# Performance work log

Hardware: AMD Instinct MI355X
Metric: run time of the kernel (lower is better)

The kernel has to match this reference:

```python
import jax, jax.numpy as jnp
import numpy as np

# DeepSeek-V3 MoE config (matches init_kwargs)
H = 1024          # hidden_size
I = 704           # moe_intermediate_size
E = 64            # n_routed_experts
TOP_K = 8         # num_experts_per_tok
NG = 8            # n_group
TOPK_GROUP = 4    # topk_group
N_SHARED = 2      # n_shared_experts
ROUTED_SCALE = 2.5
S_I = I * N_SHARED  # shared expert intermediate size


def setup_inputs() -> dict:
    key = jax.random.key(0)
    ks = jax.random.split(key, 10)
    sc = 0.02
    return {
        "hidden_states": jax.random.normal(ks[0], (1, 1024, H), dtype=jnp.float32),
        "gate_w": sc * jax.random.normal(ks[1], (E, H), dtype=jnp.float32),
        "gate_bias": sc * jax.random.normal(ks[2], (E,), dtype=jnp.float32),  # e_score_correction_bias
        "Wg": sc * jax.random.normal(ks[3], (E, I, H), dtype=jnp.float32),
        "Wu": sc * jax.random.normal(ks[4], (E, I, H), dtype=jnp.float32),
        "Wd": sc * jax.random.normal(ks[5], (E, H, I), dtype=jnp.float32),
        "Sg": sc * jax.random.normal(ks[6], (S_I, H), dtype=jnp.float32),
        "Su": sc * jax.random.normal(ks[7], (S_I, H), dtype=jnp.float32),
        "Sd": sc * jax.random.normal(ks[8], (H, S_I), dtype=jnp.float32),
    }


def _route(x, gate_w, gate_bias):
    # x: [T, H] -> dense routing weight matrix [T, E]
    T = x.shape[0]
    logits = x @ gate_w.T                         # [T, E] (fp32, as HF casts to float32)
    scores = jax.nn.sigmoid(logits)
    scores_for_choice = scores + gate_bias[None, :]
    # group scores: sum of top-2 expert scores in each group
    grp = scores_for_choice.reshape(T, NG, E // NG)
    group_scores = jnp.sum(jax.lax.top_k(grp, 2)[0], axis=-1)      # [T, NG]
    _, gidx = jax.lax.top_k(group_scores, TOPK_GROUP)              # [T, TOPK_GROUP]
    gmask = jnp.zeros((T, NG), dtype=scores.dtype).at[
        jnp.arange(T)[:, None], gidx].set(1.0)                      # [T, NG]
    emask = jnp.repeat(gmask, E // NG, axis=1)                      # [T, E]
    masked = jnp.where(emask > 0, scores_for_choice, 0.0)
    _, topk_idx = jax.lax.top_k(masked, TOP_K)                      # [T, TOP_K]
    topk_w = jnp.take_along_axis(scores, topk_idx, axis=1)          # gather from UNbiased scores
    topk_w = topk_w / (jnp.sum(topk_w, axis=-1, keepdims=True) + 1e-20)  # norm_topk_prob
    topk_w = topk_w * ROUTED_SCALE
    # dense [T, E] combine weights (zeros for unrouted experts)
    rw = jnp.zeros((T, E), dtype=scores.dtype).at[
        jnp.arange(T)[:, None], topk_idx].add(topk_w)
    return rw


def _mlp(x, gw, uw, dw):
    # SwiGLU MLP: down(silu(gate(x)) * up(x)), no biases
    return (jax.nn.silu(x @ gw.T) * (x @ uw.T)) @ dw.T


def reference(hidden_states, gate_w, gate_bias, Wg, Wu, Wd, Sg, Su, Sd):
    B, S, _ = hidden_states.shape
    x = hidden_states.reshape(B * S, H)                 # [T, H]
    rw = _route(x, gate_w, gate_bias)                   # [T, E]
    # dense reference: run every expert on every token, weighted combine
    expert_out = jax.vmap(lambda gw_, uw_, dw_: _mlp(x, gw_, uw_, dw_))(Wg, Wu, Wd)  # [E, T, H]
    routed = jnp.einsum('eth,te->th', expert_out, rw)   # [T, H]
    shared = _mlp(x, Sg, Su, Sd)                        # [T, H]
    out = (routed + shared).reshape(B, S, H)
    return out
```

## Files before the change

### kernel.cpp

```cpp
#include <hip/hip_runtime.h>
#include <hip/hip_bf16.h>
#include <cstdint>
#include <cstddef>

#define T_TOK 1024
#define H_DIM 1024
#define I_DIM 704
#define E_NUM 64
#define TOPK 8
#define NGRP 8
#define GSIZE 8
#define TOPKG 4
#define SI_DIM 1408
#define RSCALE 2.5f
#define NSLOT (T_TOK * TOPK)
#define MAXBLK 128

#define AP 72

typedef short bf16x8 __attribute__((ext_vector_type(8)));
typedef float f32x4 __attribute__((ext_vector_type(4)));

__device__ inline unsigned pk2(float x, float y) {
    __hip_bfloat162 h2 = __float22bfloat162_rn(make_float2(x, y));
    unsigned u; __builtin_memcpy(&u, &h2, 4); return u;
}
__device__ inline unsigned short bf1(float x) {
    __hip_bfloat16 h = __float2bfloat16(x);
    unsigned short u; __builtin_memcpy(&u, &h, 2); return u;
}

__global__ __launch_bounds__(64) void route_kernel(
    const float* __restrict__ x, const float* __restrict__ gw, const float* __restrict__ gb,
    int* __restrict__ counts, int* __restrict__ tk_idx, float* __restrict__ tk_w)
{
    const int t = blockIdx.x;
    __shared__ float xs[H_DIM];
    __shared__ float raw[E_NUM];
    __shared__ float sc[E_NUM];
    __shared__ float masked[E_NUM];
    __shared__ float gsc[NGRP];
    const int tid = threadIdx.x;

    const float4* xrow = (const float4*)(x + (size_t)t * H_DIM);
    for (int i = tid; i < H_DIM / 4; i += 64) ((float4*)xs)[i] = xrow[i];
    __syncthreads();

    float a = 0.f;
    const float* w = gw + (size_t)tid * H_DIM;
    for (int h = 0; h < H_DIM; h += 4) {
        float4 w4 = *(const float4*)(w + h);
        a += xs[h] * w4.x + xs[h+1] * w4.y + xs[h+2] * w4.z + xs[h+3] * w4.w;
    }
    float s = 1.f / (1.f + expf(-a));
    raw[tid] = s;
    sc[tid] = s + gb[tid];
    __syncthreads();

    if (tid == 0) {
        for (int g = 0; g < NGRP; ++g) {
            float m1 = -1e30f, m2 = -1e30f;
            for (int j = 0; j < GSIZE; ++j) {
                float v = sc[g * GSIZE + j];
                if (v > m1) { m2 = m1; m1 = v; }
                else if (v > m2) { m2 = v; }
            }
            gsc[g] = m1 + m2;
        }
        bool gsel[NGRP];
        for (int g = 0; g < NGRP; ++g) gsel[g] = false;
        for (int k = 0; k < TOPKG; ++k) {
            int best = -1; float bv = -1e30f;
            for (int g = 0; g < NGRP; ++g)
                if (!gsel[g] && gsc[g] > bv) { bv = gsc[g]; best = g; }
            gsel[best] = true;
        }
        for (int e = 0; e < E_NUM; ++e)
            masked[e] = gsel[e / GSIZE] ? sc[e] : 0.0f;
        int idx[TOPK];
        float wsum = 0.f;
        for (int k = 0; k < TOPK; ++k) {
            int best = 0; float bv = -1e30f;
            for (int e = 0; e < E_NUM; ++e)
                if (masked[e] > bv) { bv = masked[e]; best = e; }
            masked[best] = -1e30f;
            idx[k] = best;
            wsum += raw[best];
        }
        float inv = RSCALE / (wsum + 1e-20f);
        for (int k = 0; k < TOPK; ++k) {
            tk_idx[t * TOPK + k] = idx[k];
            tk_w[t * TOPK + k] = raw[idx[k]] * inv;
            atomicAdd(&counts[idx[k]], 1);
        }
    }
}

__global__ void zero_kernel(int* counts, int* fillc)
{
    int i = threadIdx.x;
    if (i < E_NUM) { counts[i] = 0; fillc[i] = 0; }
}

__global__ void scan_kernel(const int* __restrict__ counts, int* __restrict__ offs,
                            int* __restrict__ blk_e, int* __restrict__ blk_s0,
                            int* __restrict__ nblk)
{
    if (threadIdx.x == 0) {
        int acc = 0;
        for (int e = 0; e < E_NUM; ++e) { offs[e] = acc; acc += counts[e]; }
        int n = 0;
        for (int e = 0; e < E_NUM; ++e)
            for (int t = 0; t < counts[e]; t += 128) { blk_e[n] = e; blk_s0[n] = t; ++n; }
        nblk[0] = n;
    }
}

__global__ void fill_kernel(const int* __restrict__ tk_idx, const float* __restrict__ tk_w,
                            const int* __restrict__ offs, int* __restrict__ fillc,
                            int* __restrict__ tok_list, float* __restrict__ w_list,
                            int* __restrict__ tk_pos)
{
    int t = blockIdx.x * blockDim.x + threadIdx.x;
    if (t >= T_TOK) return;
    for (int k = 0; k < TOPK; ++k) {
        int e = tk_idx[t * TOPK + k];
        int pos = offs[e] + atomicAdd(&fillc[e], 1);
        tok_list[pos] = t;
        w_list[pos] = tk_w[t * TOPK + k];
        tk_pos[t * TOPK + k] = pos;
    }
}

__global__ __launch_bounds__(256) void gateup_routed_mfma(
    const float* __restrict__ x, const float* __restrict__ Wg, const float* __restrict__ Wu,
    const int* __restrict__ offs, const int* __restrict__ counts,
    const int* __restrict__ tok_list, const float* __restrict__ w_list,
    const int* __restrict__ blk_e, const int* __restrict__ blk_s0, const int* __restrict__ nblk,
    unsigned short* __restrict__ act)
{
    const int by = blockIdx.y;
    if (by >= nblk[0]) return;
    const int e = blk_e[by];
    const int m0 = blk_s0[by];
    const int cnt = counts[e];
    const int off = offs[e];
    const int n0 = blockIdx.x * 64;

    __shared__ unsigned short As[128 * AP];
    __shared__ unsigned short Bg[64 * AP];
    __shared__ unsigned short Bu[64 * AP];
    __shared__ int toks[128];
    __shared__ float wts[128];

    const int tid = threadIdx.x;
    if (tid < 128) {
        int s = m0 + tid;
        toks[tid] = (s < cnt) ? tok_list[off + s] : -1;
        wts[tid]  = (s < cnt) ? w_list[off + s] : 0.f;
    }
    __syncthreads();

    const int lane = tid & 63;
    const int wv = tid >> 6;
    const int lr = lane & 15;
    const int lq = lane >> 4;

    f32x4 accg[2][4], accu[2][4];
    #pragma unroll
    for (int i = 0; i < 2; ++i)
        #pragma unroll
        for (int j = 0; j < 4; ++j) {
            accg[i][j] = (f32x4){0.f, 0.f, 0.f, 0.f};
            accu[i][j] = (f32x4){0.f, 0.f, 0.f, 0.f};
        }

    const float* wgp = Wg + (size_t)e * I_DIM * H_DIM + (size_t)n0 * H_DIM;
    const float* wup = Wu + (size_t)e * I_DIM * H_DIM + (size_t)n0 * H_DIM;

    const int ar = tid >> 4;
    const int ac = (tid & 15) * 4;

    for (int k0 = 0; k0 < H_DIM; k0 += 64) {
        #pragma unroll
        for (int p = 0; p < 8; ++p) {
            int r = ar + p * 16;
            int tkn = toks[r];
            float4 v = make_float4(0.f, 0.f, 0.f, 0.f);
            if (tkn >= 0) v = *(const float4*)(x + (size_t)tkn * H_DIM + k0 + ac);
            *(uint2*)&As[r * AP + ac] = make_uint2(pk2(v.x, v.y), pk2(v.z, v.w));
        }
        #pragma unroll
        for (int p = 0; p < 4; ++p) {
            int r = ar + p * 16;
            float4 g = *(const float4*)(wgp + (size_t)r * H_DIM + k0 + ac);
            *(uint2*)&Bg[r * AP + ac] = make_uint2(pk2(g.x, g.y), pk2(g.z, g.w));
            float4 u = *(const float4*)(wup + (size_t)r * H_DIM + k0 + ac);
            *(uint2*)&Bu[r * AP + ac] = make_uint2(pk2(u.x, u.y), pk2(u.z, u.w));
        }
        __syncthreads();
        #pragma unroll
        for (int ks = 0; ks < 2; ++ks) {
            bf16x8 a0 = *(const bf16x8*)&As[(wv * 32 + lr) * AP + ks * 32 + lq * 8];
            bf16x8 a1 = *(const bf16x8*)&As[(wv * 32 + 16 + lr) * AP + ks * 32 + lq * 8];
            #pragma unroll
            for (int nj = 0; nj < 4; ++nj) {
                bf16x8 bg = *(const bf16x8*)&Bg[(nj * 16 + lr) * AP + ks * 32 + lq * 8];
                bf16x8 bu = *(const bf16x8*)&Bu[(nj * 16 + lr) * AP + ks * 32 + lq * 8];
                accg[0][nj] = __builtin_amdgcn_mfma_f32_16x16x32_bf16(a0, bg, accg[0][nj], 0, 0, 0);
                accg[1][nj] = __builtin_amdgcn_mfma_f32_16x16x32_bf16(a1, bg, accg[1][nj], 0, 0, 0);
                accu[0][nj] = __builtin_amdgcn_mfma_f32_16x16x32_bf16(a0, bu, accu[0][nj], 0, 0, 0);
                accu[1][nj] = __builtin_amdgcn_mfma_f32_16x16x32_bf16(a1, bu, accu[1][nj], 0, 0, 0);
            }
        }
        __syncthreads();
    }

    #pragma unroll
    for (int mi = 0; mi < 2; ++mi) {
        #pragma unroll
        for (int r = 0; r < 4; ++r) {
            int srow = wv * 32 + mi * 16 + lq * 4 + r;
            if (m0 + srow < cnt) {
                float w = wts[srow];
                unsigned short* ap = act + (size_t)(off + m0 + srow) * I_DIM + n0 + lr;
                #pragma unroll
                for (int nj = 0; nj < 4; ++nj) {
                    float g = accg[mi][nj][r];
                    float u = accu[mi][nj][r];
                    float a = w * (g / (1.f + __expf(-g))) * u;
                    ap[nj * 16] = bf1(a);
                }
            }
        }
    }
}

__global__ __launch_bounds__(256) void down_routed_mfma(
    const unsigned short* __restrict__ act, const float* __restrict__ Wd,
    const int* __restrict__ offs, const int* __restrict__ counts,
    const int* __restrict__ blk_e, const int* __restrict__ blk_s0, const int* __restrict__ nblk,
    float* __restrict__ slot_out)
{
    const int by = blockIdx.y;
    if (by >= nblk[0]) return;
    const int e = blk_e[by];
    const int m0 = blk_s0[by];
    const int cnt = counts[e];
    const int off = offs[e];
    const int n0 = blockIdx.x * 64;

    __shared__ unsigned short As[128 * AP];
    __shared__ unsigned short Bs[64 * AP];

    const int tid = threadIdx.x;
    const int lane = tid & 63;
    const int wv = tid >> 6;
    const int lr = lane & 15;
    const int lq = lane >> 4;

    f32x4 acc[2][4];
    #pragma unroll
    for (int i = 0; i < 2; ++i)
        #pragma unroll
        for (int j = 0; j < 4; ++j)
            acc[i][j] = (f32x4){0.f, 0.f, 0.f, 0.f};

    const float* wdp = Wd + (size_t)e * H_DIM * I_DIM + (size_t)n0 * I_DIM;
    const unsigned short* ap0 = act + (size_t)(off + m0) * I_DIM;
    const int ar = tid >> 4;
    const int ac = (tid & 15) * 4;

    for (int k0 = 0; k0 < I_DIM; k0 += 64) {
        #pragma unroll
        for (int p = 0; p < 8; ++p) {
            int r = ar + p * 16;
            uint2 v = make_uint2(0u, 0u);
            if (m0 + r < cnt) v = *(const uint2*)(ap0 + (size_t)r * I_DIM + k0 + ac);
            *(uint2*)&As[r * AP + ac] = v;
        }
        #pragma unroll
        for (int p = 0; p < 4; ++p) {
            int r = ar + p * 16;
            float4 w4 = *(const float4*)(wdp + (size_t)r * I_DIM + k0 + ac);
            *(uint2*)&Bs[r * AP + ac] = make_uint2(pk2(w4.x, w4.y), pk2(w4.z, w4.w));
        }
        __syncthreads();
        #pragma unroll
        for (int ks = 0; ks < 2; ++ks) {
            bf16x8 a0 = *(const bf16x8*)&As[(wv * 32 + lr) * AP + ks * 32 + lq * 8];
            bf16x8 a1 = *(const bf16x8*)&As[(wv * 32 + 16 + lr) * AP + ks * 32 + lq * 8];
            #pragma unroll
            for (int nj = 0; nj < 4; ++nj) {
                bf16x8 b = *(const bf16x8*)&Bs[(nj * 16 + lr) * AP + ks * 32 + lq * 8];
                acc[0][nj] = __builtin_amdgcn_mfma_f32_16x16x32_bf16(a0, b, acc[0][nj], 0, 0, 0);
                acc[1][nj] = __builtin_amdgcn_mfma_f32_16x16x32_bf16(a1, b, acc[1][nj], 0, 0, 0);
            }
        }
        __syncthreads();
    }

    #pragma unroll
    for (int mi = 0; mi < 2; ++mi) {
        #pragma unroll
        for (int r = 0; r < 4; ++r) {
            int srow = wv * 32 + mi * 16 + lq * 4 + r;
            if (m0 + srow < cnt) {
                float* op = slot_out + (size_t)(off + m0 + srow) * H_DIM + n0 + lr;
                #pragma unroll
                for (int nj = 0; nj < 4; ++nj)
                    op[nj * 16] = acc[mi][nj][r];
            }
        }
    }
}

__global__ __launch_bounds__(256) void combine_kernel(
    const float* __restrict__ slot_out, const int* __restrict__ tk_pos,
    float* __restrict__ out)
{
    const int t = blockIdx.x;
    __shared__ int pos[TOPK];
    if (threadIdx.x < TOPK) pos[threadIdx.x] = tk_pos[t * TOPK + threadIdx.x];
    __syncthreads();
    const int i = threadIdx.x;
    float4 a = ((const float4*)(out + (size_t)t * H_DIM))[i];
    #pragma unroll
    for (int k = 0; k < TOPK; ++k) {
        float4 v = ((const float4*)(slot_out + (size_t)pos[k] * H_DIM))[i];
        a.x += v.x; a.y += v.y; a.z += v.z; a.w += v.w;
    }
    ((float4*)(out + (size_t)t * H_DIM))[i] = a;
}

__global__ __launch_bounds__(256) void gateup_shared_mfma(
    const float* __restrict__ x, const float* __restrict__ Sg, const float* __restrict__ Su,
    unsigned short* __restrict__ sact)
{
    const int m0 = blockIdx.y * 128;
    const int n0 = blockIdx.x * 64;

    __shared__ unsigned short As[128 * AP];
    __shared__ unsigned short Bg[64 * AP];
    __shared__ unsigned short Bu[64 * AP];

    const int tid = threadIdx.x;
    const int lane = tid & 63;
    const int wv = tid >> 6;
    const int lr = lane & 15;
    const int lq = lane >> 4;

    f32x4 accg[2][4], accu[2][4];
    #pragma unroll
    for (int i = 0; i < 2; ++i)
        #pragma unroll
        for (int j = 0; j < 4; ++j) {
            accg[i][j] = (f32x4){0.f, 0.f, 0.f, 0.f};
            accu[i][j] = (f32x4){0.f, 0.f, 0.f, 0.f};
        }

    const float* gp = Sg + (size_t)n0 * H_DIM;
    const float* up = Su + (size_t)n0 * H_DIM;
    const int ar = tid >> 4;
    const int ac = (tid & 15) * 4;

    for (int k0 = 0; k0 < H_DIM; k0 += 64) {
        #pragma unroll
        for (int p = 0; p < 8; ++p) {
            int r = ar + p * 16;
            float4 v = *(const float4*)(x + (size_t)(m0 + r) * H_DIM + k0 + ac);
            *(uint2*)&As[r * AP + ac] = make_uint2(pk2(v.x, v.y), pk2(v.z, v.w));
        }
        #pragma unroll
        for (int p = 0; p < 4; ++p) {
            int r = ar + p * 16;
            float4 g = *(const float4*)(gp + (size_t)r * H_DIM + k0 + ac);
            *(uint2*)&Bg[r * AP + ac] = make_uint2(pk2(g.x, g.y), pk2(g.z, g.w));
            float4 u = *(const float4*)(up + (size_t)r * H_DIM + k0 + ac);
            *(uint2*)&Bu[r * AP + ac] = make_uint2(pk2(u.x, u.y), pk2(u.z, u.w));
        }
        __syncthreads();
        #pragma unroll
        for (int ks = 0; ks < 2; ++ks) {
            bf16x8 a0 = *(const bf16x8*)&As[(wv * 32 + lr) * AP + ks * 32 + lq * 8];
            bf16x8 a1 = *(const bf16x8*)&As[(wv * 32 + 16 + lr) * AP + ks * 32 + lq * 8];
            #pragma unroll
            for (int nj = 0; nj < 4; ++nj) {
                bf16x8 bg = *(const bf16x8*)&Bg[(nj * 16 + lr) * AP + ks * 32 + lq * 8];
                bf16x8 bu = *(const bf16x8*)&Bu[(nj * 16 + lr) * AP + ks * 32 + lq * 8];
                accg[0][nj] = __builtin_amdgcn_mfma_f32_16x16x32_bf16(a0, bg, accg[0][nj], 0, 0, 0);
                accg[1][nj] = __builtin_amdgcn_mfma_f32_16x16x32_bf16(a1, bg, accg[1][nj], 0, 0, 0);
                accu[0][nj] = __builtin_amdgcn_mfma_f32_16x16x32_bf16(a0, bu, accu[0][nj], 0, 0, 0);
                accu[1][nj] = __builtin_amdgcn_mfma_f32_16x16x32_bf16(a1, bu, accu[1][nj], 0, 0, 0);
            }
        }
        __syncthreads();
    }

    #pragma unroll
    for (int mi = 0; mi < 2; ++mi) {
        #pragma unroll
        for (int r = 0; r < 4; ++r) {
            int trow = m0 + wv * 32 + mi * 16 + lq * 4 + r;
            unsigned short* sp = sact + (size_t)trow * SI_DIM + n0 + lr;
            #pragma unroll
            for (int nj = 0; nj < 4; ++nj) {
                float g = accg[mi][nj][r];
                float u = accu[mi][nj][r];
                float a = (g / (1.f + __expf(-g))) * u;
                sp[nj * 16] = bf1(a);
            }
        }
    }
}

__global__ __launch_bounds__(256) void down_shared_mfma(
    const unsigned short* __restrict__ sact, const float* __restrict__ Sd,
    float* __restrict__ out)
{
    const int m0 = blockIdx.y * 128;
    const int n0 = blockIdx.x * 64;

    __shared__ unsigned short As[128 * AP];
    __shared__ unsigned short Bs[64 * AP];

    const int tid = threadIdx.x;
    const int lane = tid & 63;
    const int wv = tid >> 6;
    const int lr = lane & 15;
    const int lq = lane >> 4;

    f32x4 acc[2][4];
    #pragma unroll
    for (int i = 0; i < 2; ++i)
        #pragma unroll
        for (int j = 0; j < 4; ++j)
            acc[i][j] = (f32x4){0.f, 0.f, 0.f, 0.f};

    const float* wp = Sd + (size_t)n0 * SI_DIM;
    const int ar = tid >> 4;
    const int ac = (tid & 15) * 4;

    for (int k0 = 0; k0 < SI_DIM; k0 += 64) {
        #pragma unroll
        for (int p = 0; p < 8; ++p) {
            int r = ar + p * 16;
            uint2 v = *(const uint2*)(sact + (size_t)(m0 + r) * SI_DIM + k0 + ac);
            *(uint2*)&As[r * AP + ac] = v;
        }
        #pragma unroll
        for (int p = 0; p < 4; ++p) {
            int r = ar + p * 16;
            float4 w4 = *(const float4*)(wp + (size_t)r * SI_DIM + k0 + ac);
            *(uint2*)&Bs[r * AP + ac] = make_uint2(pk2(w4.x, w4.y), pk2(w4.z, w4.w));
        }
        __syncthreads();
        #pragma unroll
        for (int ks = 0; ks < 2; ++ks) {
            bf16x8 a0 = *(const bf16x8*)&As[(wv * 32 + lr) * AP + ks * 32 + lq * 8];
            bf16x8 a1 = *(const bf16x8*)&As[(wv * 32 + 16 + lr) * AP + ks * 32 + lq * 8];
            #pragma unroll
            for (int nj = 0; nj < 4; ++nj) {
                bf16x8 b = *(const bf16x8*)&Bs[(nj * 16 + lr) * AP + ks * 32 + lq * 8];
                acc[0][nj] = __builtin_amdgcn_mfma_f32_16x16x32_bf16(a0, b, acc[0][nj], 0, 0, 0);
                acc[1][nj] = __builtin_amdgcn_mfma_f32_16x16x32_bf16(a1, b, acc[1][nj], 0, 0, 0);
            }
        }
        __syncthreads();
    }

    #pragma unroll
    for (int mi = 0; mi < 2; ++mi) {
        #pragma unroll
        for (int r = 0; r < 4; ++r) {
            int trow = m0 + wv * 32 + mi * 16 + lq * 4 + r;
            float* op = out + (size_t)trow * H_DIM + n0 + lr;
            #pragma unroll
            for (int nj = 0; nj < 4; ++nj)
                op[nj * 16] = acc[mi][nj][r];
        }
    }
}

extern "C" void kernel_launch(void* const* d_in, const int* in_sizes, int n_in,
                              void* d_out, int out_size, void* d_ws, size_t ws_size,
                              hipStream_t stream)
{
    const float* x  = (const float*)d_in[0];
    const float* gw = (const float*)d_in[1];
    const float* gb = (const float*)d_in[2];
    const float* Wg = (const float*)d_in[3];
    const float* Wu = (const float*)d_in[4];
    const float* Wd = (const float*)d_in[5];
    const float* Sg = (const float*)d_in[6];
    const float* Su = (const float*)d_in[7];
    const float* Sd = (const float*)d_in[8];
    float* out = (float*)d_out;

    float* slot_out = (float*)d_ws;
    unsigned short* act  = (unsigned short*)(slot_out + (size_t)NSLOT * H_DIM);
    unsigned short* sact = act + (size_t)NSLOT * I_DIM;
    int* counts   = (int*)(sact + (size_t)T_TOK * SI_DIM);
    int* fillc    = counts + 64;
    int* offs     = fillc + 64;
    int* tk_idx   = offs + 64;
    float* tk_w   = (float*)(tk_idx + NSLOT);
    int* tok_list = (int*)(tk_w + NSLOT);
    float* w_list = (float*)(tok_list + NSLOT);
    int* tk_pos   = (int*)(w_list + NSLOT);
    int* blk_e    = tk_pos + NSLOT;
    int* blk_s0   = blk_e + MAXBLK;
    int* nblk     = blk_s0 + MAXBLK;

    zero_kernel<<<1, 64, 0, stream>>>(counts, fillc);
    route_kernel<<<T_TOK, 64, 0, stream>>>(x, gw, gb, counts, tk_idx, tk_w);
    scan_kernel<<<1, 64, 0, stream>>>(counts, offs, blk_e, blk_s0, nblk);
    fill_kernel<<<4, 256, 0, stream>>>(tk_idx, tk_w, offs, fillc, tok_list, w_list, tk_pos);

    gateup_routed_mfma<<<dim3(11, MAXBLK), 256, 0, stream>>>(
        x, Wg, Wu, offs, counts, tok_list, w_list, blk_e, blk_s0, nblk, act);
    gateup_shared_mfma<<<dim3(22, 8), 256, 0, stream>>>(x, Sg, Su, sact);
    down_shared_mfma<<<dim3(16, 8), 256, 0, stream>>>(sact, Sd, out);
    down_routed_mfma<<<dim3(16, MAXBLK), 256, 0, stream>>>(
        act, Wd, offs, counts, blk_e, blk_s0, nblk, slot_out);
    combine_kernel<<<T_TOK, 256, 0, stream>>>(slot_out, tk_pos, out);
}
```

Baseline: 808.2 us.

## Fold shared expert into routed grouped GEMM as two virtual experts

Treats the shared expert MLP as two extra virtual experts, each taking one half of the 1408 intermediate size and every token with weight 1. The shared expert then runs inside the same grouped gate/up and down kernels, and its outputs are summed in the combine kernel, which removes two separate launches. The GEMM blocks also grow from 256 to 512 threads, with each wave computing a 16-row slice instead of 32. This adds slot_out and act workspace for 2048 extra slots, and it adds extra reads in combine.

```diff
diff --git a/kernel.cpp b/kernel.cpp
--- a/kernel.cpp
+++ b/kernel.cpp
@@ -14,7 +14,9 @@
 #define SI_DIM 1408
 #define RSCALE 2.5f
 #define NSLOT (T_TOK * TOPK)
-#define MAXBLK 128
+#define NSLOT2 (NSLOT + 2 * T_TOK)
+#define EV_NUM (E_NUM + 2)
+#define MAXBLK 160
 
 #define AP 72
 
@@ -100,6 +102,7 @@
 {
     int i = threadIdx.x;
     if (i < E_NUM) { counts[i] = 0; fillc[i] = 0; }
+    if (i >= E_NUM && i < EV_NUM) counts[i] = T_TOK;
 }
 
 __global__ void scan_kernel(const int* __restrict__ counts, int* __restrict__ offs,
@@ -109,8 +112,10 @@
     if (threadIdx.x == 0) {
         int acc = 0;
         for (int e = 0; e < E_NUM; ++e) { offs[e] = acc; acc += counts[e]; }
+        offs[E_NUM]     = NSLOT;
+        offs[E_NUM + 1] = NSLOT + T_TOK;
         int n = 0;
-        for (int e = 0; e < E_NUM; ++e)
+        for (int e = 0; e < EV_NUM; ++e)
             for (int t = 0; t < counts[e]; t += 128) { blk_e[n] = e; blk_s0[n] = t; ++n; }
         nblk[0] = n;
     }
@@ -130,10 +135,13 @@
         w_list[pos] = tk_w[t * TOPK + k];
         tk_pos[t * TOPK + k] = pos;
     }
-}
-
-__global__ __launch_bounds__(256) void gateup_routed_mfma(
+    tok_list[NSLOT + t] = t;          w_list[NSLOT + t] = 1.f;
+    tok_list[NSLOT + T_TOK + t] = t;  w_list[NSLOT + T_TOK + t] = 1.f;
+}
+
+__global__ __launch_bounds__(512) void gateup_mfma(
     const float* __restrict__ x, const float* __restrict__ Wg, const float* __restrict__ Wu,
+    const float* __restrict__ Sg, const float* __restrict__ Su,
     const int* __restrict__ offs, const int* __restrict__ counts,
     const int* __restrict__ tok_list, const float* __restrict__ w_list,
     const int* __restrict__ blk_e, const int* __restrict__ blk_s0, const int* __restrict__ nblk,
@@ -166,33 +174,35 @@
     const int lr = lane & 15;
     const int lq = lane >> 4;
 
-    f32x4 accg[2][4], accu[2][4];
-    #pragma unroll
-    for (int i = 0; i < 2; ++i)
-        #pragma unroll
-        for (int j = 0; j < 4; ++j) {
-            accg[i][j] = (f32x4){0.f, 0.f, 0.f, 0.f};
-            accu[i][j] = (f32x4){0.f, 0.f, 0.f, 0.f};
-        }
-
-    const float* wgp = Wg + (size_t)e * I_DIM * H_DIM + (size_t)n0 * H_DIM;
-    const float* wup = Wu + (size_t)e * I_DIM * H_DIM + (size_t)n0 * H_DIM;
+    f32x4 accg[4], accu[4];
+    #pragma unroll
+    for (int j = 0; j < 4; ++j) {
+        accg[j] = (f32x4){0.f, 0.f, 0.f, 0.f};
+        accu[j] = (f32x4){0.f, 0.f, 0.f, 0.f};
+    }
+
+    const float* wgp = (e < E_NUM)
+        ? Wg + (size_t)e * I_DIM * H_DIM + (size_t)n0 * H_DIM
+        : Sg + (size_t)(e - E_NUM) * I_DIM * H_DIM + (size_t)n0 * H_DIM;
+    const float* wup = (e < E_NUM)
+        ? Wu + (size_t)e * I_DIM * H_DIM + (size_t)n0 * H_DIM
+        : Su + (size_t)(e - E_NUM) * I_DIM * H_DIM + (size_t)n0 * H_DIM;
 
     const int ar = tid >> 4;
     const int ac = (tid & 15) * 4;
 
     for (int k0 = 0; k0 < H_DIM; k0 += 64) {
         #pragma unroll
-        for (int p = 0; p < 8; ++p) {
-            int r = ar + p * 16;
+        for (int p = 0; p < 4; ++p) {
+            int r = ar + p * 32;
             int tkn = toks[r];
             float4 v = make_float4(0.f, 0.f, 0.f, 0.f);
             if (tkn >= 0) v = *(const float4*)(x + (size_t)tkn * H_DIM + k0 + ac);
             *(uint2*)&As[r * AP + ac] = make_uint2(pk2(v.x, v.y), pk2(v.z, v.w));
         }
         #pragma unroll
-        for (int p = 0; p < 4; ++p) {
-            int r = ar + p * 16;
+        for (int p = 0; p < 2; ++p) {
+            int r = ar + p * 32;
             float4 g = *(const float4*)(wgp + (size_t)r * H_DIM + k0 + ac);
             *(uint2*)&Bg[r * AP + ac] = make_uint2(pk2(g.x, g.y), pk2(g.z, g.w));
             float4 u = *(const float4*)(wup + (size_t)r * H_DIM + k0 + ac);
@@ -201,43 +211,38 @@
         __syncthreads();
         #pragma unroll
         for (int ks = 0; ks < 2; ++ks) {
-            bf16x8 a0 = *(const bf16x8*)&As[(wv * 32 + lr) * AP + ks * 32 + lq * 8];
-            bf16x8 a1 = *(const bf16x8*)&As[(wv * 32 + 16 + lr) * AP + ks * 32 + lq * 8];
+            bf16x8 a = *(const bf16x8*)&As[(wv * 16 + lr) * AP + ks * 32 + lq * 8];
             #pragma unroll
             for (int nj = 0; nj < 4; ++nj) {
                 bf16x8 bg = *(const bf16x8*)&Bg[(nj * 16 + lr) * AP + ks * 32 + lq * 8];
                 bf16x8 bu = *(const bf16x8*)&Bu[(nj * 16 + lr) * AP + ks * 32 + lq * 8];
-                accg[0][nj] = __builtin_amdgcn_mfma_f32_16x16x32_bf16(a0, bg, accg[0][nj], 0, 0, 0);
-                accg[1][nj] = __builtin_amdgcn_mfma_f32_16x16x32_bf16(a1, bg, accg[1][nj], 0, 0, 0);
-                accu[0][nj] = __builtin_amdgcn_mfma_f32_16x16x32_bf16(a0, bu, accu[0][nj], 0, 0, 0);
-                accu[1][nj] = __builtin_amdgcn_mfma_f32_16x16x32_bf16(a1, bu, accu[1][nj], 0, 0, 0);
+                accg[nj] = __builtin_amdgcn_mfma_f32_16x16x32_bf16(a, bg, accg[nj], 0, 0, 0);
+                accu[nj] = __builtin_amdgcn_mfma_f32_16x16x32_bf16(a, bu, accu[nj], 0, 0, 0);
             }
         }
         __syncthreads();
     }
 
     #pragma unroll
-    for (int mi = 0; mi < 2; ++mi) {
-        #pragma unroll
-        for (int r = 0; r < 4; ++r) {
-            int srow = wv * 32 + mi * 16 + lq * 4 + r;
-            if (m0 + srow < cnt) {
-                float w = wts[srow];
-                unsigned short* ap = act + (size_t)(off + m0 + srow) * I_DIM + n0 + lr;
-                #pragma unroll
-                for (int nj = 0; nj < 4; ++nj) {
-                    float g = accg[mi][nj][r];
-                    float u = accu[mi][nj][r];
-                    float a = w * (g / (1.f + __expf(-g))) * u;
-                    ap[nj * 16] = bf1(a);
-                }
+    for (int r = 0; r < 4; ++r) {
+        int srow = wv * 16 + lq * 4 + r;
+        if (m0 + srow < cnt) {
+            float w = wts[srow];
+            unsigned short* ap = act + (size_t)(off + m0 + srow) * I_DIM + n0 + lr;
+            #pragma unroll
+            for (int nj = 0; nj < 4; ++nj) {
+                float g = accg[nj][r];
+                float u = accu[nj][r];
+                float a = w * (g / (1.f + __expf(-g))) * u;
+                ap[nj * 16] = bf1(a);
             }
         }
     }
 }
 
-__global__ __launch_bounds__(256) void down_routed_mfma(
+__global__ __launch_bounds__(512) void down_mfma(
     const unsigned short* __restrict__ act, const float* __restrict__ Wd,
+    const float* __restrict__ Sd,
     const int* __restrict__ offs, const int* __restrict__ counts,
     const int* __restrict__ blk_e, const int* __restrict__ blk_s0, const int* __restrict__ nblk,
     float* __restrict__ slot_out)
@@ -259,58 +264,59 @@
     const int lr = lane & 15;
     const int lq = lane >> 4;
 
-    f32x4 acc[2][4];
-    #pragma unroll
-    for (int i = 0; i < 2; ++i)
-        #pragma unroll
-        for (int j = 0; j < 4; ++j)
-            acc[i][j] = (f32x4){0.f, 0.f, 0.f, 0.f};
-
-    const float* wdp = Wd + (size_t)e * H_DIM * I_DIM + (size_t)n0 * I_DIM;
+    f32x4 acc[4];
+    #pragma unroll
+    for (int j = 0; j < 4; ++j)
+        acc[j] = (f32x4){0.f, 0.f, 0.f, 0.f};
+
+    const float* wdp;
+    size_t wpitch;
+    if (e < E_NUM) {
+        wdp = Wd + (size_t)e * H_DIM * I_DIM + (size_t)n0 * I_DIM;
+        wpitch = I_DIM;
+    } else {
+        wdp = Sd + (size_t)n0 * SI_DIM + (size_t)(e - E_NUM) * I_DIM;
+        wpitch = SI_DIM;
+    }
     const unsigned short* ap0 = act + (size_t)(off + m0) * I_DIM;
     const int ar = tid >> 4;
     const int ac = (tid & 15) * 4;
 
     for (int k0 = 0; k0 < I_DIM; k0 += 64) {
         #pragma unroll
-        for (int p = 0; p < 8; ++p) {
-            int r = ar + p * 16;
+        for (int p = 0; p < 4; ++p) {
+            int r = ar + p * 32;
             uint2 v = make_uint2(0u, 0u);
             if (m0 + r < cnt) v = *(const uint2*)(ap0 + (size_t)r * I_DIM + k0 + ac);
             *(uint2*)&As[r * AP + ac] = v;
         }
         #pragma unroll
-        for (int p = 0; p < 4; ++p) {
-            int r = ar + p * 16;
-            float4 w4 = *(const float4*)(wdp + (size_t)r * I_DIM + k0 + ac);
+        for (int p = 0; p < 2; ++p) {
+            int r = ar + p * 32;
+            float4 w4 = *(const float4*)(wdp + (size_t)r * wpitch + k0 + ac);
             *(uint2*)&Bs[r * AP + ac] = make_uint2(pk2(w4.x, w4.y), pk2(w4.z, w4.w));
         }
         __syncthreads();
         #pragma unroll
         for (int ks = 0; ks < 2; ++ks) {
-            bf16x8 a0 = *(const bf16x8*)&As[(wv * 32 + lr) * AP + ks * 32 + lq * 8];
-            bf16x8 a1 = *(const bf16x8*)&As[(wv * 32 + 16 + lr) * AP + ks * 32 + lq * 8];
+            bf16x8 a = *(const bf16x8*)&As[(wv * 16 + lr) * AP + ks * 32 + lq * 8];
             #pragma unroll
             for (int nj = 0; nj < 4; ++nj) {
                 bf16x8 b = *(const bf16x8*)&Bs[(nj * 16 + lr) * AP + ks * 32 + lq * 8];
-                acc[0][nj] = __builtin_amdgcn_mfma_f32_16x16x32_bf16(a0, b, acc[0][nj], 0, 0, 0);
-                acc[1][nj] = __builtin_amdgcn_mfma_f32_16x16x32_bf16(a1, b, acc[1][nj], 0, 0, 0);
+                acc[nj] = __builtin_amdgcn_mfma_f32_16x16x32_bf16(a, b, acc[nj], 0, 0, 0);
             }
         }
         __syncthreads();
     }
 
     #pragma unroll
-    for (int mi = 0; mi < 2; ++mi) {
-        #pragma unroll
-        for (int r = 0; r < 4; ++r) {
-            int srow = wv * 32 + mi * 16 + lq * 4 + r;
-            if (m0 + srow < cnt) {
-                float* op = slot_out + (size_t)(off + m0 + srow) * H_DIM + n0 + lr;
-                #pragma unroll
-                for (int nj = 0; nj < 4; ++nj)
-                    op[nj * 16] = acc[mi][nj][r];
-            }
+    for (int r = 0; r < 4; ++r) {
+        int srow = wv * 16 + lq * 4 + r;
+        if (m0 + srow < cnt) {
+            float* op = slot_out + (size_t)(off + m0 + srow) * H_DIM + n0 + lr;
+            #pragma unroll
+            for (int nj = 0; nj < 4; ++nj)
+                op[nj * 16] = acc[nj][r];
         }
     }
 }
@@ -320,166 +326,19 @@
     float* __restrict__ out)
 {
     const int t = blockIdx.x;
-    __shared__ int pos[TOPK];
+    __shared__ int pos[TOPK + 2];
     if (threadIdx.x < TOPK) pos[threadIdx.x] = tk_pos[t * TOPK + threadIdx.x];
+    else if (threadIdx.x == TOPK)     pos[TOPK]     = NSLOT + t;
+    else if (threadIdx.x == TOPK + 1) pos[TOPK + 1] = NSLOT + T_TOK + t;
     __syncthreads();
     const int i = threadIdx.x;
-    float4 a = ((const float4*)(out + (size_t)t * H_DIM))[i];
-    #pragma unroll
-    for (int k = 0; k < TOPK; ++k) {
+    float4 a = make_float4(0.f, 0.f, 0.f, 0.f);
+    #pragma unroll
+    for (int k = 0; k < TOPK + 2; ++k) {
         float4 v = ((const float4*)(slot_out + (size_t)pos[k] * H_DIM))[i];
         a.x += v.x; a.y += v.y; a.z += v.z; a.w += v.w;
     }
     ((float4*)(out + (size_t)t * H_DIM))[i] = a;
-}
-
-__global__ __launch_bounds__(256) void gateup_shared_mfma(
-    const float* __restrict__ x, const float* __restrict__ Sg, const float* __restrict__ Su,
-    unsigned short* __restrict__ sact)
-{
-    const int m0 = blockIdx.y * 128;
-    const int n0 = blockIdx.x * 64;
-
-    __shared__ unsigned short As[128 * AP];
-    __shared__ unsigned short Bg[64 * AP];
-    __shared__ unsigned short Bu[64 * AP];
-
-    const int tid = threadIdx.x;
-    const int lane = tid & 63;
-    const int wv = tid >> 6;
-    const int lr = lane & 15;
-    const int lq = lane >> 4;
-
-    f32x4 accg[2][4], accu[2][4];
-    #pragma unroll
-    for (int i = 0; i < 2; ++i)
-        #pragma unroll
-        for (int j = 0; j < 4; ++j) {
-            accg[i][j] = (f32x4){0.f, 0.f, 0.f, 0.f};
-            accu[i][j] = (f32x4){0.f, 0.f, 0.f, 0.f};
-        }
-
-    const float* gp = Sg + (size_t)n0 * H_DIM;
-    const float* up = Su + (size_t)n0 * H_DIM;
-    const int ar = tid >> 4;
-    const int ac = (tid & 15) * 4;
-
-    for (int k0 = 0; k0 < H_DIM; k0 += 64) {
-        #pragma unroll
-        for (int p = 0; p < 8; ++p) {
-            int r = ar + p * 16;
-            float4 v = *(const float4*)(x + (size_t)(m0 + r) * H_DIM + k0 + ac);
-            *(uint2*)&As[r * AP + ac] = make_uint2(pk2(v.x, v.y), pk2(v.z, v.w));
-        }
-        #pragma unroll
-        for (int p = 0; p < 4; ++p) {
-            int r = ar + p * 16;
-            float4 g = *(const float4*)(gp + (size_t)r * H_DIM + k0 + ac);
-            *(uint2*)&Bg[r * AP + ac] = make_uint2(pk2(g.x, g.y), pk2(g.z, g.w));
-            float4 u = *(const float4*)(up + (size_t)r * H_DIM + k0 + ac);
-            *(uint2*)&Bu[r * AP + ac] = make_uint2(pk2(u.x, u.y), pk2(u.z, u.w));
-        }
-        __syncthreads();
-        #pragma unroll
-        for (int ks = 0; ks < 2; ++ks) {
-            bf16x8 a0 = *(const bf16x8*)&As[(wv * 32 + lr) * AP + ks * 32 + lq * 8];
-            bf16x8 a1 = *(const bf16x8*)&As[(wv * 32 + 16 + lr) * AP + ks * 32 + lq * 8];
-            #pragma unroll
-            for (int nj = 0; nj < 4; ++nj) {
-                bf16x8 bg = *(const bf16x8*)&Bg[(nj * 16 + lr) * AP + ks * 32 + lq * 8];
-                bf16x8 bu = *(const bf16x8*)&Bu[(nj * 16 + lr) * AP + ks * 32 + lq * 8];
-                accg[0][nj] = __builtin_amdgcn_mfma_f32_16x16x32_bf16(a0, bg, accg[0][nj], 0, 0, 0);
-                accg[1][nj] = __builtin_amdgcn_mfma_f32_16x16x32_bf16(a1, bg, accg[1][nj], 0, 0, 0);
-                accu[0][nj] = __builtin_amdgcn_mfma_f32_16x16x32_bf16(a0, bu, accu[0][nj], 0, 0, 0);
-                accu[1][nj] = __builtin_amdgcn_mfma_f32_16x16x32_bf16(a1, bu, accu[1][nj], 0, 0, 0);
-            }
-        }
-        __syncthreads();
-    }
-
-    #pragma unroll
-    for (int mi = 0; mi < 2; ++mi) {
-        #pragma unroll
-        for (int r = 0; r < 4; ++r) {
-            int trow = m0 + wv * 32 + mi * 16 + lq * 4 + r;
-            unsigned short* sp = sact + (size_t)trow * SI_DIM + n0 + lr;
-            #pragma unroll
-            for (int nj = 0; nj < 4; ++nj) {
-                float g = accg[mi][nj][r];
-                float u = accu[mi][nj][r];
-                float a = (g / (1.f + __expf(-g))) * u;
-                sp[nj * 16] = bf1(a);
-            }
-        }
-    }
-}
-
-__global__ __launch_bounds__(256) void down_shared_mfma(
-    const unsigned short* __restrict__ sact, const float* __restrict__ Sd,
-    float* __restrict__ out)
-{
-    const int m0 = blockIdx.y * 128;
-    const int n0 = blockIdx.x * 64;
-
-    __shared__ unsigned short As[128 * AP];
-    __shared__ unsigned short Bs[64 * AP];
-
-    const int tid = threadIdx.x;
-    const int lane = tid & 63;
-    const int wv = tid >> 6;
-    const int lr = lane & 15;
-    const int lq = lane >> 4;
-
-    f32x4 acc[2][4];
-    #pragma unroll
-    for (int i = 0; i < 2; ++i)
-        #pragma unroll
-        for (int j = 0; j < 4; ++j)
-            acc[i][j] = (f32x4){0.f, 0.f, 0.f, 0.f};
-
-    const float* wp = Sd + (size_t)n0 * SI_DIM;
-    const int ar = tid >> 4;
-    const int ac = (tid & 15) * 4;
-
-    for (int k0 = 0; k0 < SI_DIM; k0 += 64) {
-        #pragma unroll
-        for (int p = 0; p < 8; ++p) {
-            int r = ar + p * 16;
-            uint2 v = *(const uint2*)(sact + (size_t)(m0 + r) * SI_DIM + k0 + ac);
-            *(uint2*)&As[r * AP + ac] = v;
-        }
-        #pragma unroll
-        for (int p = 0; p < 4; ++p) {
-            int r = ar + p * 16;
-            float4 w4 = *(const float4*)(wp + (size_t)r * SI_DIM + k0 + ac);
-            *(uint2*)&Bs[r * AP + ac] = make_uint2(pk2(w4.x, w4.y), pk2(w4.z, w4.w));
-        }
-        __syncthreads();
-        #pragma unroll
-        for (int ks = 0; ks < 2; ++ks) {
-            bf16x8 a0 = *(const bf16x8*)&As[(wv * 32 + lr) * AP + ks * 32 + lq * 8];
-            bf16x8 a1 = *(const bf16x8*)&As[(wv * 32 + 16 + lr) * AP + ks * 32 + lq * 8];
-            #pragma unroll
-            for (int nj = 0; nj < 4; ++nj) {
-                bf16x8 b = *(const bf16x8*)&Bs[(nj * 16 + lr) * AP + ks * 32 + lq * 8];
-                acc[0][nj] = __builtin_amdgcn_mfma_f32_16x16x32_bf16(a0, b, acc[0][nj], 0, 0, 0);
-                acc[1][nj] = __builtin_amdgcn_mfma_f32_16x16x32_bf16(a1, b, acc[1][nj], 0, 0, 0);
-            }
-        }
-        __syncthreads();
-    }
-
-    #pragma unroll
-    for (int mi = 0; mi < 2; ++mi) {
-        #pragma unroll
-        for (int r = 0; r < 4; ++r) {
-            int trow = m0 + wv * 32 + mi * 16 + lq * 4 + r;
-            float* op = out + (size_t)trow * H_DIM + n0 + lr;
-            #pragma unroll
-            for (int nj = 0; nj < 4; ++nj)
-                op[nj * 16] = acc[mi][nj][r];
-        }
-    }
 }
 
 extern "C" void kernel_launch(void* const* d_in, const int* in_sizes, int n_in,
@@ -498,30 +357,27 @@
     float* out = (float*)d_out;
 
     float* slot_out = (float*)d_ws;
-    unsigned short* act  = (unsigned short*)(slot_out + (size_t)NSLOT * H_DIM);
-    unsigned short* sact = act + (size_t)NSLOT * I_DIM;
-    int* counts   = (int*)(sact + (size_t)T_TOK * SI_DIM);
-    int* fillc    = counts + 64;
+    unsigned short* act  = (unsigned short*)(slot_out + (size_t)NSLOT2 * H_DIM);
+    int* counts   = (int*)(act + (size_t)NSLOT2 * I_DIM);
+    int* fillc    = counts + EV_NUM;
     int* offs     = fillc + 64;
-    int* tk_idx   = offs + 64;
+    int* tk_idx   = offs + EV_NUM;
     float* tk_w   = (float*)(tk_idx + NSLOT);
     int* tok_list = (int*)(tk_w + NSLOT);
-    float* w_list = (float*)(tok_list + NSLOT);
-    int* tk_pos   = (int*)(w_list + NSLOT);
+    float* w_list = (float*)(tok_list + NSLOT2);
+    int* tk_pos   = (int*)(w_list + NSLOT2);
     int* blk_e    = tk_pos + NSLOT;
     int* blk_s0   = blk_e + MAXBLK;
     int* nblk     = blk_s0 + MAXBLK;
 
-    zero_kernel<<<1, 64, 0, stream>>>(counts, fillc);
+    zero_kernel<<<1, 128, 0, stream>>>(counts, fillc);
     route_kernel<<<T_TOK, 64, 0, stream>>>(x, gw, gb, counts, tk_idx, tk_w);
     scan_kernel<<<1, 64, 0, stream>>>(counts, offs, blk_e, blk_s0, nblk);
     fill_kernel<<<4, 256, 0, stream>>>(tk_idx, tk_w, offs, fillc, tok_list, w_list, tk_pos);
 
-    gateup_routed_mfma<<<dim3(11, MAXBLK), 256, 0, stream>>>(
-        x, Wg, Wu, offs, counts, tok_list, w_list, blk_e, blk_s0, nblk, act);
-    gateup_shared_mfma<<<dim3(22, 8), 256, 0, stream>>>(x, Sg, Su, sact);
-    down_shared_mfma<<<dim3(16, 8), 256, 0, stream>>>(sact, Sd, out);
-    down_routed_mfma<<<dim3(16, MAXBLK), 256, 0, stream>>>(
-        act, Wd, offs, counts, blk_e, blk_s0, nblk, slot_out);
+    gateup_mfma<<<dim3(11, MAXBLK), 512, 0, stream>>>(
+        x, Wg, Wu, Sg, Su, offs, counts, tok_list, w_list, blk_e, blk_s0, nblk, act);
+    down_mfma<<<dim3(16, MAXBLK), 512, 0, stream>>>(
+        act, Wd, Sd, offs, counts, blk_e, blk_s0, nblk, slot_out);
     combine_kernel<<<T_TOK, 256, 0, stream>>>(slot_out, tk_pos, out);
 }
```

Result: faster. 729.1 us (-9.8%).
